# Kernel tuning notes

Hardware: AMD Instinct MI355X
Metric: run time of the kernel (lower is better)

The kernel has to match this reference:

```python
import jax, jax.numpy as jnp
import numpy as np

B, C, H, K = 1024, 1000, 768, 128

def setup_inputs() -> dict:
    key = jax.random.key(0)
    k1, k2, k3, k4 = jax.random.split(key, 4)
    x = jax.random.normal(k1, (B, H), dtype=jnp.float32)
    y = jax.random.randint(k2, (B,), 0, C)
    class_weights = jax.random.normal(k3, (C, H, K), dtype=jnp.float32) * 0.1
    class_bias = jnp.zeros((C, H), dtype=jnp.float32)
    # torch.nn.Linear default init (uniform in +/- 1/sqrt(H))
    bound = 1.0 / np.sqrt(H)
    W_lin = jax.random.uniform(k4, (H, H), dtype=jnp.float32, minval=-bound, maxval=bound)
    b_lin = jnp.zeros((H,), dtype=jnp.float32)
    return {"x": x, "y": y, "class_weights": class_weights,
            "class_bias": class_bias, "W_lin": W_lin, "b_lin": b_lin}

def reference(x, y, class_weights, class_bias, W_lin, b_lin):
    # one-hot matmul gather == true indexed gather (same math)
    weights = class_weights[y]                # [B, H, K]
    neg_x = jax.nn.relu(-x)                   # [B, H]
    x1 = jnp.tanh(neg_x @ W_lin.T + b_lin)    # [B, H]
    # x1[B,1,H] @ weights[B,H,K] -> sum over singleton dim == [B, K]
    logits = jnp.einsum('bh,bhk->bk', x1, weights)
    return logits
```

## Files before the change

kernel.cpp:

```cpp
#include <hip/hip_runtime.h>
#include <cstddef>

#define B_SZ 1024
#define C_SZ 1000
#define H_SZ 768
#define K_SZ 128

__global__ __launch_bounds__(256) void gemm_relu_tanh(
    const float* __restrict__ x, const float* __restrict__ W,
    const float* __restrict__ bias, float* __restrict__ x1)
{
    const int TM = 64, TN = 64, BK = 16;
    __shared__ float As[BK][TM];
    __shared__ float Bs[BK][TN];

    const int t    = threadIdx.x;
    const int row0 = blockIdx.y * TM;
    const int col0 = blockIdx.x * TN;
    const int tx   = t & 15;
    const int ty   = t >> 4;

    const int lk = (t & 3) * 4;
    const int lm = t >> 2;

    float acc[4][4] = {};

    for (int k0 = 0; k0 < H_SZ; k0 += BK) {
        float4 a4 = *(const float4*)(x + (size_t)(row0 + lm) * H_SZ + k0 + lk);
        As[lk + 0][lm] = fmaxf(-a4.x, 0.f);
        As[lk + 1][lm] = fmaxf(-a4.y, 0.f);
        As[lk + 2][lm] = fmaxf(-a4.z, 0.f);
        As[lk + 3][lm] = fmaxf(-a4.w, 0.f);
        float4 b4 = *(const float4*)(W + (size_t)(col0 + lm) * H_SZ + k0 + lk);
        Bs[lk + 0][lm] = b4.x;
        Bs[lk + 1][lm] = b4.y;
        Bs[lk + 2][lm] = b4.z;
        Bs[lk + 3][lm] = b4.w;
        __syncthreads();

        #pragma unroll
        for (int k = 0; k < BK; ++k) {
            float av[4], bv[4];
            #pragma unroll
            for (int i = 0; i < 4; ++i) av[i] = As[k][ty * 4 + i];
            #pragma unroll
            for (int j = 0; j < 4; ++j) bv[j] = Bs[k][tx * 4 + j];
            #pragma unroll
            for (int i = 0; i < 4; ++i)
                #pragma unroll
                for (int j = 0; j < 4; ++j)
                    acc[i][j] += av[i] * bv[j];
        }
        __syncthreads();
    }

    #pragma unroll
    for (int i = 0; i < 4; ++i) {
        const int m = row0 + ty * 4 + i;
        #pragma unroll
        for (int j = 0; j < 4; ++j) {
            const int n = col0 + tx * 4 + j;
            x1[(size_t)m * H_SZ + n] = tanhf(acc[i][j] + bias[n]);
        }
    }
}

__global__ __launch_bounds__(256) void gather_dot(
    const float* __restrict__ x1, const int* __restrict__ y,
    const float* __restrict__ cw, float* __restrict__ out)
{
    const int b   = blockIdx.x;
    const int t   = threadIdx.x;
    const int k4  = t & 31;
    const int hg  = t >> 5;

    __shared__ float sx[H_SZ];
    __shared__ float4 red[256];

    const int cls = y[b];
    const float4* __restrict__ wrow =
        (const float4*)(cw + (size_t)cls * H_SZ * K_SZ);

    for (int i = t; i < H_SZ; i += 256)
        sx[i] = x1[(size_t)b * H_SZ + i];
    __syncthreads();

    float4 acc = {0.f, 0.f, 0.f, 0.f};
    #pragma unroll 4
    for (int h = hg; h < H_SZ; h += 8) {
        const float  xv = sx[h];
        const float4 w  = wrow[h * 32 + k4];
        acc.x += xv * w.x;
        acc.y += xv * w.y;
        acc.z += xv * w.z;
        acc.w += xv * w.w;
    }

    red[t] = acc;
    __syncthreads();
    if (t < 128) {
        float4 o = red[t + 128];
        red[t].x += o.x; red[t].y += o.y; red[t].z += o.z; red[t].w += o.w;
    }
    __syncthreads();
    if (t < 64) {
        float4 o = red[t + 64];
        red[t].x += o.x; red[t].y += o.y; red[t].z += o.z; red[t].w += o.w;
    }
    __syncthreads();
    if (t < 32) {
        float4 r = red[t];
        float4 o = red[t + 32];
        r.x += o.x; r.y += o.y; r.z += o.z; r.w += o.w;
        ((float4*)out)[(size_t)b * 32 + t] = r;
    }
}

extern "C" void kernel_launch(void* const* d_in, const int* in_sizes, int n_in,
                              void* d_out, int out_size, void* d_ws, size_t ws_size,
                              hipStream_t stream) {
    const float* x    = (const float*)d_in[0];
    const int*   y    = (const int*)  d_in[1];
    const float* cw   = (const float*)d_in[2];
    const float* Wlin = (const float*)d_in[4];
    const float* blin = (const float*)d_in[5];
    float* out = (float*)d_out;
    float* x1  = (float*)d_ws;

    dim3 g1(H_SZ / 64, B_SZ / 64);
    gemm_relu_tanh<<<g1, 256, 0, stream>>>(x, Wlin, blin, x1);
    gather_dot<<<B_SZ, 256, 0, stream>>>(x1, y, cw, out);
}
```

Before: 546.7 us.

## Convert GEMM inputs to bf16 and use MFMA for relu-linear-tanh stage

Adds a pre-pass kernel that applies relu(-x) and converts x and W_lin to bf16 in workspace, then replaces the fp32 scalar-FMA tiled GEMM with a bf16 MFMA 16x16x32 kernel that keeps the fused bias and tanh epilogue. The goal is to cut the compute time of the dense B x H x H matmul by running it on the matrix cores. In exchange it adds an extra launch and a round trip through memory for the converted operands, and bf16 inputs reduce precision. The gather_dot stage, which likely dominates because it reads large class-weight slices, is left unchanged.

```diff
diff --git a/kernel.cpp b/kernel.cpp
--- a/kernel.cpp
+++ b/kernel.cpp
@@ -1,4 +1,5 @@
 #include <hip/hip_runtime.h>
+#include <hip/hip_bf16.h>
 #include <cstddef>
 
 #define B_SZ 1024
@@ -6,61 +7,99 @@
 #define H_SZ 768
 #define K_SZ 128
 
-__global__ __launch_bounds__(256) void gemm_relu_tanh(
+typedef __attribute__((ext_vector_type(8))) short bf16x8;
+typedef __attribute__((ext_vector_type(4))) float f32x4;
+
+#define WS_NEGX_OFF 0
+#define WS_W_OFF    1572864
+#define WS_X1_OFF   4194304
+
+__global__ __launch_bounds__(256) void convert_pack(
     const float* __restrict__ x, const float* __restrict__ W,
+    ushort* __restrict__ negx, ushort* __restrict__ Wb)
+{
+    const int NX = B_SZ * H_SZ / 4;
+    const int NW = H_SZ * H_SZ / 4;
+    int i = blockIdx.x * 256 + threadIdx.x;
+    if (i < NX) {
+        float4 v = ((const float4*)x)[i];
+        union { ushort u[4]; ushort4 v4; } o;
+        o.u[0] = __bfloat16_as_ushort(__float2bfloat16(fmaxf(-v.x, 0.f)));
+        o.u[1] = __bfloat16_as_ushort(__float2bfloat16(fmaxf(-v.y, 0.f)));
+        o.u[2] = __bfloat16_as_ushort(__float2bfloat16(fmaxf(-v.z, 0.f)));
+        o.u[3] = __bfloat16_as_ushort(__float2bfloat16(fmaxf(-v.w, 0.f)));
+        ((ushort4*)negx)[i] = o.v4;
+    } else {
+        int j = i - NX;
+        if (j < NW) {
+            float4 v = ((const float4*)W)[j];
+            union { ushort u[4]; ushort4 v4; } o;
+            o.u[0] = __bfloat16_as_ushort(__float2bfloat16(v.x));
+            o.u[1] = __bfloat16_as_ushort(__float2bfloat16(v.y));
+            o.u[2] = __bfloat16_as_ushort(__float2bfloat16(v.z));
+            o.u[3] = __bfloat16_as_ushort(__float2bfloat16(v.w));
+            ((ushort4*)Wb)[j] = o.v4;
+        }
+    }
+}
+
+__global__ __launch_bounds__(256) void mfma_gemm_tanh(
+    const ushort* __restrict__ A, const ushort* __restrict__ Bw,
     const float* __restrict__ bias, float* __restrict__ x1)
 {
-    const int TM = 64, TN = 64, BK = 16;
-    __shared__ float As[BK][TM];
-    __shared__ float Bs[BK][TN];
+    const int LDA = 40;
+    __shared__ ushort sA[64 * LDA];
+    __shared__ ushort sB[64 * LDA];
 
     const int t    = threadIdx.x;
-    const int row0 = blockIdx.y * TM;
-    const int col0 = blockIdx.x * TN;
-    const int tx   = t & 15;
-    const int ty   = t >> 4;
+    const int wave = t >> 6;
+    const int lane = t & 63;
+    const int wm   = wave >> 1;
+    const int wn   = wave & 1;
+    const int m0   = blockIdx.y * 64;
+    const int n0   = blockIdx.x * 64;
 
-    const int lk = (t & 3) * 4;
-    const int lm = t >> 2;
+    const int lr = t >> 2;
+    const int lc = (t & 3) * 8;
 
-    float acc[4][4] = {};
+    f32x4 acc[2][2] = {};
 
-    for (int k0 = 0; k0 < H_SZ; k0 += BK) {
-        float4 a4 = *(const float4*)(x + (size_t)(row0 + lm) * H_SZ + k0 + lk);
-        As[lk + 0][lm] = fmaxf(-a4.x, 0.f);
-        As[lk + 1][lm] = fmaxf(-a4.y, 0.f);
-        As[lk + 2][lm] = fmaxf(-a4.z, 0.f);
-        As[lk + 3][lm] = fmaxf(-a4.w, 0.f);
-        float4 b4 = *(const float4*)(W + (size_t)(col0 + lm) * H_SZ + k0 + lk);
-        Bs[lk + 0][lm] = b4.x;
-        Bs[lk + 1][lm] = b4.y;
-        Bs[lk + 2][lm] = b4.z;
-        Bs[lk + 3][lm] = b4.w;
+    const int fr = lane & 15;
+    const int fk = (lane >> 4) * 8;
+
+    for (int k0 = 0; k0 < H_SZ; k0 += 32) {
+        *(bf16x8*)(&sA[lr * LDA + lc]) =
+            *(const bf16x8*)(&A[(size_t)(m0 + lr) * H_SZ + k0 + lc]);
+        *(bf16x8*)(&sB[lr * LDA + lc]) =
+            *(const bf16x8*)(&Bw[(size_t)(n0 + lr) * H_SZ + k0 + lc]);
         __syncthreads();
 
         #pragma unroll
-        for (int k = 0; k < BK; ++k) {
-            float av[4], bv[4];
+        for (int fi = 0; fi < 2; ++fi) {
+            bf16x8 af = *(const bf16x8*)(&sA[(wm * 32 + fi * 16 + fr) * LDA + fk]);
             #pragma unroll
-            for (int i = 0; i < 4; ++i) av[i] = As[k][ty * 4 + i];
-            #pragma unroll
-            for (int j = 0; j < 4; ++j) bv[j] = Bs[k][tx * 4 + j];
-            #pragma unroll
-            for (int i = 0; i < 4; ++i)
-                #pragma unroll
-                for (int j = 0; j < 4; ++j)
-                    acc[i][j] += av[i] * bv[j];
+            for (int fj = 0; fj < 2; ++fj) {
+                bf16x8 bf = *(const bf16x8*)(&sB[(wn * 32 + fj * 16 + fr) * LDA + fk]);
+                acc[fi][fj] = __builtin_amdgcn_mfma_f32_16x16x32_bf16(
+                    af, bf, acc[fi][fj], 0, 0, 0);
+            }
         }
         __syncthreads();
     }
 
+    const int col   = lane & 15;
+    const int rbase = (lane >> 4) * 4;
     #pragma unroll
-    for (int i = 0; i < 4; ++i) {
-        const int m = row0 + ty * 4 + i;
+    for (int fi = 0; fi < 2; ++fi) {
         #pragma unroll
-        for (int j = 0; j < 4; ++j) {
-            const int n = col0 + tx * 4 + j;
-            x1[(size_t)m * H_SZ + n] = tanhf(acc[i][j] + bias[n]);
+        for (int fj = 0; fj < 2; ++fj) {
+            const int n  = n0 + wn * 32 + fj * 16 + col;
+            const float bv = bias[n];
+            #pragma unroll
+            for (int r = 0; r < 4; ++r) {
+                const int m = m0 + wm * 32 + fi * 16 + rbase + r;
+                x1[(size_t)m * H_SZ + n] = tanhf(acc[fi][fj][r] + bv);
+            }
         }
     }
 }
@@ -125,9 +164,17 @@
     const float* Wlin = (const float*)d_in[4];
     const float* blin = (const float*)d_in[5];
     float* out = (float*)d_out;
-    float* x1  = (float*)d_ws;
+
+    char* ws = (char*)d_ws;
+    ushort* negx = (ushort*)(ws + WS_NEGX_OFF);
+    ushort* Wb   = (ushort*)(ws + WS_W_OFF);
+    float*  x1   = (float*) (ws + WS_X1_OFF);
+
+    const int total4 = (B_SZ * H_SZ + H_SZ * H_SZ) / 4;
+    convert_pack<<<(total4 + 255) / 256, 256, 0, stream>>>(x, Wlin, negx, Wb);
 
     dim3 g1(H_SZ / 64, B_SZ / 64);
-    gemm_relu_tanh<<<g1, 256, 0, stream>>>(x, Wlin, blin, x1);
+    mfma_gemm_tanh<<<g1, 256, 0, stream>>>(negx, Wb, blin, x1);
+
     gather_dot<<<B_SZ, 256, 0, stream>>>(x1, y, cw, out);
 }
```

After: 511.4 us. 1.07x faster.
